# Optimization experiments

Measured on AMD Instinct MI355X. Metric: run time of the kernel, lower is better.

## Reference

```python
import jax, jax.numpy as jnp
import numpy as np

D_MODEL = 1024
NUM_HEADS = 16
HEAD_DIM = D_MODEL // NUM_HEADS
SCALE = 1.0 / float(np.sqrt(HEAD_DIM))


def setup_inputs() -> dict:
    key = jax.random.key(0)
    ks = jax.random.split(key, 9)
    B, S, D = 2, 2048, D_MODEL
    # Xavier-uniform bound for square (D, D) linear layers
    bound = float(np.sqrt(6.0 / (D + D)))
    def xavier(k):
        return jax.random.uniform(k, (D, D), jnp.float32, -bound, bound)
    return {
        "x": jax.random.normal(ks[0], (B, S, D), jnp.float32),
        "Wq": xavier(ks[1]), "bq": jnp.zeros((D,), jnp.float32),
        "Wk": xavier(ks[2]), "bk": jnp.zeros((D,), jnp.float32),
        "Wv": xavier(ks[3]), "bv": jnp.zeros((D,), jnp.float32),
        "Wo": xavier(ks[4]), "bo": jnp.zeros((D,), jnp.float32),
    }


def reference(x, Wq, bq, Wk, bk, Wv, bv, Wo, bo):
    B, S, D = x.shape
    H, Hd = NUM_HEADS, HEAD_DIM
    # torch Linear: y = x @ W.T + b
    def proj(W, b):
        y = jnp.einsum("bsd,ed->bse", x, W) + b
        return y.reshape(B, S, H, Hd).transpose(0, 2, 1, 3)  # (B,H,S,Hd)
    Q = proj(Wq, bq)
    K = proj(Wk, bk)
    V = proj(Wv, bv)
    # scaled scores (B,H,S,S) + additive causal mask (0 / -inf)
    scores = jnp.einsum("bhqd,bhkd->bhqk", Q, K) * SCALE
    causal = jnp.where(
        jnp.tril(jnp.ones((S, S), dtype=bool)), 0.0, -jnp.inf
    ).astype(scores.dtype)
    scores = scores + causal
    attn = jax.nn.softmax(scores, axis=-1)
    attn = jnp.nan_to_num(attn, nan=0.0)  # no-op here (causal rows never fully masked)
    # dropout p=0.0 -> identity
    ctx = jnp.einsum("bhqk,bhkd->bhqd", attn, V)  # (B,H,S,Hd)
    ctx = ctx.transpose(0, 2, 1, 3).reshape(B, S, D)
    out = jnp.einsum("bsd,ed->bse", ctx, Wo) + bo
    return out, attn
```

## Files before the change

### kernel.cpp

```cpp
#include <hip/hip_runtime.h>

typedef unsigned short u16;
using short8 = __attribute__((ext_vector_type(8))) short;
using f32x4  = __attribute__((ext_vector_type(4))) float;
using u16x4  = __attribute__((ext_vector_type(4))) unsigned short;

__device__ __forceinline__ u16 f2bf(float f) {
  union { float f; unsigned int u; } v; v.f = f;
  unsigned int u = v.u + 0x7FFFu + ((v.u >> 16) & 1u);
  return (u16)(u >> 16);
}
__device__ __forceinline__ float bf2f(u16 u) {
  union { unsigned int u; float f; } v; v.u = ((unsigned int)u) << 16;
  return v.f;
}
__device__ __forceinline__ void glds16(const void* g, void* l) {
  __builtin_amdgcn_global_load_lds(
      (const __attribute__((address_space(1))) void*)g,
      (__attribute__((address_space(3))) void*)l, 16, 0, 0);
}

__global__ __launch_bounds__(256) void cast_all(
    const float* __restrict__ x, const float* __restrict__ wq,
    const float* __restrict__ wk, const float* __restrict__ wv,
    const float* __restrict__ wo,
    u16* __restrict__ xb, u16* __restrict__ wqb, u16* __restrict__ wkb,
    u16* __restrict__ wvb, u16* __restrict__ wob) {
  int i = blockIdx.x * 256 + threadIdx.x;
  const float4* src; ushort4* dst; int off;
  if (i < 1048576)      { src = (const float4*)x;  dst = (ushort4*)xb;  off = i; }
  else if (i < 1310720) { src = (const float4*)wq; dst = (ushort4*)wqb; off = i - 1048576; }
  else if (i < 1572864) { src = (const float4*)wk; dst = (ushort4*)wkb; off = i - 1310720; }
  else if (i < 1835008) { src = (const float4*)wv; dst = (ushort4*)wvb; off = i - 1572864; }
  else                  { src = (const float4*)wo; dst = (ushort4*)wob; off = i - 1835008; }
  float4 v = src[off];
  ushort4 o;
  o.x = f2bf(v.x); o.y = f2bf(v.y); o.z = f2bf(v.z); o.w = f2bf(v.w);
  dst[off] = o;
}

template<int MODE>
__global__ __launch_bounds__(256) void gemm_nt_glds(
    const u16* __restrict__ A,
    const u16* __restrict__ B0, const u16* __restrict__ B1, const u16* __restrict__ B2,
    const float* __restrict__ bias0, const float* __restrict__ bias1, const float* __restrict__ bias2,
    void* __restrict__ C0, void* __restrict__ C1, void* __restrict__ C2,
    int K)
{
  __shared__ u16 smem[16896];
  u16* As = smem;
  u16* Bs = smem + 8192;
  const int bn = blockIdx.x, bm = blockIdx.y;
  const int sel = bn >> 3, bnl = bn & 7;
  const u16* B = sel == 0 ? B0 : (sel == 1 ? B1 : B2);
  const float* bias = sel == 0 ? bias0 : (sel == 1 ? bias1 : bias2);
  void* C = sel == 0 ? C0 : (sel == 1 ? C1 : C2);

  const int tid = threadIdx.x;
  const int w = tid >> 6, lane = tid & 63, quad = lane >> 4, l16 = lane & 15;
  const int wm = w >> 1, wn = w & 1;
  const int srow = lane >> 3, gc = (lane & 7) ^ srow;

  const u16* aseg = A + (size_t)(bm * 128 + w * 32 + srow) * K + gc * 8;
  const u16* bseg = B + (size_t)(bnl * 128 + w * 32 + srow) * K + gc * 8;

  const f32x4 z4 = {0.f, 0.f, 0.f, 0.f};
  f32x4 acc[4][4];
#pragma unroll
  for (int mt = 0; mt < 4; mt++)
#pragma unroll
    for (int nt = 0; nt < 4; nt++) acc[mt][nt] = z4;

  for (int k0 = 0; k0 < K; k0 += 64) {
    __syncthreads();
#pragma unroll
    for (int j = 0; j < 4; j++) {
      glds16(aseg + (size_t)(j * 8) * K + k0, As + (w * 4 + j) * 512);
      glds16(bseg + (size_t)(j * 8) * K + k0, Bs + (w * 4 + j) * 512);
    }
    __syncthreads();
#pragma unroll
    for (int ks = 0; ks < 2; ks++) {
      short8 af[4], bf[4];
#pragma unroll
      for (int mt = 0; mt < 4; mt++) {
        int row = wm * 64 + mt * 16 + l16;
        int chk = (ks * 4 + quad) ^ (row & 7);
        af[mt] = *(const short8*)((const short*)As + row * 64 + chk * 8);
      }
#pragma unroll
      for (int nt = 0; nt < 4; nt++) {
        int row = wn * 64 + nt * 16 + l16;
        int chk = (ks * 4 + quad) ^ (row & 7);
        bf[nt] = *(const short8*)((const short*)Bs + row * 64 + chk * 8);
      }
#pragma unroll
      for (int mt = 0; mt < 4; mt++)
#pragma unroll
        for (int nt = 0; nt < 4; nt++)
          acc[mt][nt] = __builtin_amdgcn_mfma_f32_16x16x32_bf16(af[mt], bf[nt], acc[mt][nt], 0, 0, 0);
    }
  }

  if (MODE == 0 && sel == 2) {
    __syncthreads();
#pragma unroll
    for (int mt = 0; mt < 4; mt++) {
      int r0 = wm * 64 + mt * 16 + quad * 4;
#pragma unroll
      for (int nt = 0; nt < 4; nt++) {
        int c = wn * 64 + nt * 16 + l16;
        float bvv = bias[bnl * 128 + c];
        u16x4 pk;
#pragma unroll
        for (int r = 0; r < 4; r++) pk[r] = f2bf(acc[mt][nt][r] + bvv);
        *(u16x4*)(smem + c * 132 + r0) = pk;
      }
    }
    __syncthreads();
    const int bb = bm >> 4;
    const size_t sb = (size_t)(bm & 15) * 128;
    u16* Cv = (u16*)C;
#pragma unroll
    for (int i = 0; i < 16; i++) {
      int idx = tid + i * 256;
      int dr = idx >> 5, c4 = (idx & 31) * 4;
      u16x4 v = *(const u16x4*)(smem + dr * 132 + c4);
      *(u16x4*)(Cv + ((size_t)bb * 1024 + bnl * 128 + dr) * 2048 + sb + c4) = v;
    }
  } else {
    const float cmul = (MODE == 0 && sel == 0) ? 0.125f : 1.0f;
#pragma unroll
    for (int mt = 0; mt < 4; mt++) {
      int row0 = bm * 128 + wm * 64 + mt * 16 + quad * 4;
#pragma unroll
      for (int nt = 0; nt < 4; nt++) {
        int col = bnl * 128 + wn * 64 + nt * 16 + l16;
        float bv = bias[col];
#pragma unroll
        for (int r = 0; r < 4; r++) {
          float v = (acc[mt][nt][r] + bv) * cmul;
          if (MODE) ((float*)C)[(size_t)(row0 + r) * 1024 + col] = v;
          else      ((u16*)C)[(size_t)(row0 + r) * 1024 + col] = f2bf(v);
        }
      }
    }
  }
}

__global__ __launch_bounds__(256) void attn_kernel(
    const u16* __restrict__ Qb, const u16* __restrict__ Kbuf,
    const u16* __restrict__ Vtb, float* __restrict__ attn,
    u16* __restrict__ ctx)
{
  __shared__ u16 Ks[2][128 * 64];
  __shared__ u16 Ps[128 * 128];
  __shared__ float ls[128];

  const int flat = blockIdx.x;
  const int half = flat >> 8, r0 = flat & 255;
  const int bh = (half << 4) | (r0 >> 4);
  const int qb = half ? (15 - (r0 & 15)) : (r0 & 15);
  const int b = bh >> 4, h = bh & 15;

  const int tid = threadIdx.x;
  const int w = tid >> 6, lane = tid & 63, quad = lane >> 4, l16 = lane & 15;
  const int wm = w >> 1, wn = w & 1;
  const int srow8 = lane >> 3, gc8 = (lane & 7) ^ srow8;
  const int srow16 = lane >> 4, sc16 = lane & 15;

  const int S = 2048, D = 1024;
  const u16* Qg = Qb + ((size_t)b * S + qb * 128) * D + h * 64;
  const u16* Kg = Kbuf + (size_t)b * S * D + h * 64;
  const u16* Vg = Vtb + ((size_t)b * D + h * 64) * S;
  float* attng = attn + ((size_t)(b * 16 + h) * S + qb * 128) * S;

  const f32x4 z4 = {0.f, 0.f, 0.f, 0.f};

#pragma unroll
  for (int j = 0; j < 4; j++)
    glds16(Qg + (size_t)(w * 32 + j * 8 + srow8) * D + gc8 * 8, (u16*)Ps + (w * 4 + j) * 512);
  if (tid < 128) ls[tid] = 0.f;
#pragma unroll
  for (int j = 0; j < 4; j++)
    glds16(Kg + (size_t)(w * 32 + j * 8 + srow8) * D + gc8 * 8, Ks[0] + (w * 4 + j) * 512);
  __syncthreads();

  short8 qf[4][2];
#pragma unroll
  for (int mt = 0; mt < 4; mt++) {
    int row = wm * 64 + mt * 16 + l16;
#pragma unroll
    for (int ks = 0; ks < 2; ks++) {
      int chk = (ks * 4 + quad) ^ (row & 7);
      qf[mt][ks] = *(const short8*)((const short*)Ps + row * 64 + chk * 8);
    }
  }

  float rowsum[4][4];
#pragma unroll
  for (int mt = 0; mt < 4; mt++)
#pragma unroll
    for (int rr = 0; rr < 4; rr++) rowsum[mt][rr] = 0.f;

  for (int kb = 0; kb <= qb; kb++) {
    if (kb) __syncthreads();
    if (kb < qb) {
#pragma unroll
      for (int j = 0; j < 4; j++)
        glds16(Kg + (size_t)((kb + 1) * 128 + w * 32 + j * 8 + srow8) * D + gc8 * 8,
               Ks[(kb + 1) & 1] + (w * 4 + j) * 512);
    }
    const u16* kbf = Ks[kb & 1];
    f32x4 acc[4][4];
#pragma unroll
    for (int mt = 0; mt < 4; mt++)
#pragma unroll
      for (int nt = 0; nt < 4; nt++) acc[mt][nt] = z4;
    __builtin_amdgcn_s_setprio(1);
#pragma unroll
    for (int ks = 0; ks < 2; ks++) {
      short8 bf[4];
#pragma unroll
      for (int nt = 0; nt < 4; nt++) {
        int row = wn * 64 + nt * 16 + l16;
        int chk = (ks * 4 + quad) ^ (row & 7);
        bf[nt] = *(const short8*)((const short*)kbf + row * 64 + chk * 8);
      }
#pragma unroll
      for (int mt = 0; mt < 4; mt++)
#pragma unroll
        for (int nt = 0; nt < 4; nt++)
          acc[mt][nt] = __builtin_amdgcn_mfma_f32_16x16x32_bf16(qf[mt][ks], bf[nt], acc[mt][nt], 0, 0, 0);
    }
    __builtin_amdgcn_s_setprio(0);
    if (kb < qb) {
#pragma unroll
      for (int mt = 0; mt < 4; mt++)
#pragma unroll
        for (int rr = 0; rr < 4; rr++) {
          float s = 0.f;
#pragma unroll
          for (int nt = 0; nt < 4; nt++)
            s += __expf(fminf(acc[mt][nt][rr], 30.f));
          rowsum[mt][rr] += s;
        }
    } else {
#pragma unroll
      for (int mt = 0; mt < 4; mt++)
#pragma unroll
        for (int rr = 0; rr < 4; rr++) {
          int rloc = wm * 64 + mt * 16 + quad * 4 + rr;
          float s = 0.f;
#pragma unroll
          for (int nt = 0; nt < 4; nt++) {
            int ck = wn * 64 + nt * 16 + l16;
            s += (ck <= rloc) ? __expf(fminf(acc[mt][nt][rr], 30.f)) : 0.f;
          }
          rowsum[mt][rr] += s;
        }
    }
  }

#pragma unroll
  for (int mt = 0; mt < 4; mt++)
#pragma unroll
    for (int rr = 0; rr < 4; rr++) {
      float s = rowsum[mt][rr];
      s += __shfl_xor(s, 1);
      s += __shfl_xor(s, 2);
      s += __shfl_xor(s, 4);
      s += __shfl_xor(s, 8);
      if (l16 == 0) atomicAdd(&ls[wm * 64 + mt * 16 + quad * 4 + rr], s);
    }
  __syncthreads();
  float rl[4][4];
#pragma unroll
  for (int mt = 0; mt < 4; mt++)
#pragma unroll
    for (int rr = 0; rr < 4; rr++)
      rl[mt][rr] = 1.0f / ls[wm * 64 + mt * 16 + quad * 4 + rr];

#pragma unroll
  for (int j = 0; j < 4; j++)
    glds16(Kg + (size_t)(w * 32 + j * 8 + srow8) * D + gc8 * 8, Ks[0] + (w * 4 + j) * 512);

  f32x4 cacc[2][4];
#pragma unroll
  for (int mt = 0; mt < 2; mt++)
#pragma unroll
    for (int nt = 0; nt < 4; nt++) cacc[mt][nt] = z4;

  for (int kb = 0; kb <= qb; kb++) {
    __syncthreads();
#pragma unroll
    for (int j = 0; j < 4; j++) {
      int r0v = (w * 4 + j) * 4;
      int row = r0v + srow16;
      int gcv = sc16 ^ (row & 7);
      glds16(Vg + (size_t)row * S + kb * 128 + gcv * 8, Ks[1] + r0v * 128);
    }
    f32x4 acc[4][4];
#pragma unroll
    for (int mt = 0; mt < 4; mt++)
#pragma unroll
      for (int nt = 0; nt < 4; nt++) acc[mt][nt] = z4;
    __builtin_amdgcn_s_setprio(1);
#pragma unroll
    for (int ks = 0; ks < 2; ks++) {
      short8 bf[4];
#pragma unroll
      for (int nt = 0; nt < 4; nt++) {
        int row = wn * 64 + nt * 16 + l16;
        int chk = (ks * 4 + quad) ^ (row & 7);
        bf[nt] = *(const short8*)((const short*)Ks[0] + row * 64 + chk * 8);
      }
#pragma unroll
      for (int mt = 0; mt < 4; mt++)
#pragma unroll
        for (int nt = 0; nt < 4; nt++)
          acc[mt][nt] = __builtin_amdgcn_mfma_f32_16x16x32_bf16(qf[mt][ks], bf[nt], acc[mt][nt], 0, 0, 0);
    }
    __builtin_amdgcn_s_setprio(0);
    bool diag = (kb == qb);
#pragma unroll
    for (int mt = 0; mt < 4; mt++)
#pragma unroll
      for (int rr = 0; rr < 4; rr++) {
        int rloc = wm * 64 + mt * 16 + quad * 4 + rr;
        float rlv = rl[mt][rr];
#pragma unroll
        for (int nt = 0; nt < 4; nt++) {
          int colk = wn * 64 + nt * 16 + l16;
          float e = __expf(fminf(acc[mt][nt][rr], 30.f)) * rlv;
          if (diag && colk > rloc) e = 0.f;
          Ps[rloc * 128 + (((colk >> 3) ^ (rloc & 7)) << 3) + (colk & 7)] = f2bf(e);
        }
      }
    __syncthreads();
    if (kb < qb) {
#pragma unroll
      for (int j = 0; j < 4; j++)
        glds16(Kg + (size_t)((kb + 1) * 128 + w * 32 + j * 8 + srow8) * D + gc8 * 8,
               Ks[0] + (w * 4 + j) * 512);
    }
#pragma unroll
    for (int s = 0; s < 16; s++) {
      int e4 = s * 256 + tid;
      int row = e4 >> 5, col = (e4 & 31) * 4;
      int chunk = (col >> 3) ^ (row & 7);
      u16x4 pv = *(const u16x4*)((const u16*)Ps + row * 128 + chunk * 8 + (col & 7));
      f32x4 o;
      o[0] = bf2f(pv[0]); o[1] = bf2f(pv[1]); o[2] = bf2f(pv[2]); o[3] = bf2f(pv[3]);
      __builtin_nontemporal_store(o, (f32x4*)(attng + (size_t)row * S + kb * 128 + col));
    }
    __builtin_amdgcn_s_setprio(1);
#pragma unroll
    for (int ks = 0; ks < 4; ks++) {
      short8 pf[2], vf[4];
#pragma unroll
      for (int mt = 0; mt < 2; mt++) {
        int row = w * 32 + mt * 16 + l16;
        int chk = (ks * 4 + quad) ^ (row & 7);
        pf[mt] = *(const short8*)((const short*)Ps + row * 128 + chk * 8);
      }
#pragma unroll
      for (int nt = 0; nt < 4; nt++) {
        int row = nt * 16 + l16;
        int chk = (ks * 4 + quad) ^ (row & 7);
        vf[nt] = *(const short8*)((const short*)Ks[1] + row * 128 + chk * 8);
      }
#pragma unroll
      for (int mt = 0; mt < 2; mt++)
#pragma unroll
        for (int nt = 0; nt < 4; nt++)
          cacc[mt][nt] = __builtin_amdgcn_mfma_f32_16x16x32_bf16(pf[mt], vf[nt], cacc[mt][nt], 0, 0, 0);
    }
    __builtin_amdgcn_s_setprio(0);
  }

  {
    int kstart = (qb + 1) * 128;
    const f32x4 zz = {0.f, 0.f, 0.f, 0.f};
    for (int rr = 0; rr < 128; rr++) {
      float* rowp = attng + (size_t)rr * S;
      for (int c = kstart + tid * 4; c < S; c += 1024)
        __builtin_nontemporal_store(zz, (f32x4*)(rowp + c));
    }
  }

#pragma unroll
  for (int mt = 0; mt < 2; mt++)
#pragma unroll
    for (int nt = 0; nt < 4; nt++)
#pragma unroll
      for (int rr = 0; rr < 4; rr++) {
        int row_local = w * 32 + mt * 16 + quad * 4 + rr;
        int col = nt * 16 + l16;
        ctx[((size_t)b * S + qb * 128 + row_local) * D + h * 64 + col] = f2bf(cacc[mt][nt][rr]);
      }
}

extern "C" void kernel_launch(void* const* d_in, const int* in_sizes, int n_in,
                              void* d_out, int out_size, void* d_ws, size_t ws_size,
                              hipStream_t stream) {
  const float* x  = (const float*)d_in[0];
  const float* Wq = (const float*)d_in[1];
  const float* bq = (const float*)d_in[2];
  const float* Wk = (const float*)d_in[3];
  const float* bk = (const float*)d_in[4];
  const float* Wv = (const float*)d_in[5];
  const float* bv = (const float*)d_in[6];
  const float* Wo = (const float*)d_in[7];
  const float* bo = (const float*)d_in[8];

  float* out_f32  = (float*)d_out;
  float* attn_out = (float*)d_out + 4194304;

  char* w = (char*)d_ws;
  u16* xb   = (u16*)(w + 0);
  u16* Wqb  = (u16*)(w + 8388608);
  u16* Wkb  = (u16*)(w + 10485760);
  u16* Wvb  = (u16*)(w + 12582912);
  u16* Wob  = (u16*)(w + 14680064);
  u16* Qbuf = (u16*)(w + 16777216);
  u16* Kbuf = (u16*)(w + 25165824);
  u16* Vtb  = (u16*)(w + 41943040);
  u16* ctxb = (u16*)(w + 50331648);

  cast_all<<<8192, 256, 0, stream>>>(x, Wq, Wk, Wv, Wo, xb, Wqb, Wkb, Wvb, Wob);

  gemm_nt_glds<0><<<dim3(24, 32), 256, 0, stream>>>(
      xb, Wqb, Wkb, Wvb, bq, bk, bv, Qbuf, Kbuf, Vtb, 1024);

  attn_kernel<<<512, 256, 0, stream>>>(Qbuf, Kbuf, Vtb, attn_out, ctxb);

  gemm_nt_glds<1><<<dim3(8, 32), 256, 0, stream>>>(
      ctxb, Wob, Wob, Wob, bo, bo, bo, out_f32, out_f32, out_f32, 1024);
}
```

Measured before the change: 713.8 us.

## Double attention block to 512 threads and remap blocks to balance causal work per XCD

The attention kernel now launches 512 threads per block with 8 waves, each wave owning 32 query rows in the score phase (4x2 wave grid) and 16 rows in the PV phase. Per-wave accumulators and loads are halved, which lowers register pressure and aims to raise latency hiding within each 128-row query tile. Block indices are also remapped so that blocks landing on the same XCD (flat & 7) get a balanced mix of ascending and descending causal tiles from the same heads. In exchange, synchronisation involves more waves, and MFMA work per LDS fragment load drops.

Measured after the change: 775.6 us. 1.09x slower.

```diff
diff --git a/kernel.cpp b/kernel.cpp
--- a/kernel.cpp
+++ b/kernel.cpp
@@ -148,7 +148,7 @@
   }
 }
 
-__global__ __launch_bounds__(256) void attn_kernel(
+__global__ __launch_bounds__(512, 4) void attn_kernel(
     const u16* __restrict__ Qb, const u16* __restrict__ Kbuf,
     const u16* __restrict__ Vtb, float* __restrict__ attn,
     u16* __restrict__ ctx)
@@ -158,9 +158,10 @@
   __shared__ float ls[128];
 
   const int flat = blockIdx.x;
-  const int half = flat >> 8, r0 = flat & 255;
-  const int bh = (half << 4) | (r0 >> 4);
-  const int qb = half ? (15 - (r0 & 15)) : (r0 & 15);
+  const int x = flat & 7, slot = flat >> 3;
+  int bh, qb;
+  if (slot < 32) { bh = x * 4 + (slot >> 4);            qb = slot & 15; }
+  else           { bh = x * 4 + 2 + ((slot - 32) >> 4); qb = 15 - ((slot - 32) & 15); }
   const int b = bh >> 4, h = bh & 15;
 
   const int tid = threadIdx.x;
@@ -178,18 +179,18 @@
   const f32x4 z4 = {0.f, 0.f, 0.f, 0.f};
 
 #pragma unroll
-  for (int j = 0; j < 4; j++)
-    glds16(Qg + (size_t)(w * 32 + j * 8 + srow8) * D + gc8 * 8, (u16*)Ps + (w * 4 + j) * 512);
+  for (int j = 0; j < 2; j++)
+    glds16(Qg + (size_t)(w * 16 + j * 8 + srow8) * D + gc8 * 8, (u16*)Ps + (w * 2 + j) * 512);
   if (tid < 128) ls[tid] = 0.f;
 #pragma unroll
-  for (int j = 0; j < 4; j++)
-    glds16(Kg + (size_t)(w * 32 + j * 8 + srow8) * D + gc8 * 8, Ks[0] + (w * 4 + j) * 512);
+  for (int j = 0; j < 2; j++)
+    glds16(Kg + (size_t)(w * 16 + j * 8 + srow8) * D + gc8 * 8, Ks[0] + (w * 2 + j) * 512);
   __syncthreads();
 
-  short8 qf[4][2];
-#pragma unroll
-  for (int mt = 0; mt < 4; mt++) {
-    int row = wm * 64 + mt * 16 + l16;
+  short8 qf[2][2];
+#pragma unroll
+  for (int mt = 0; mt < 2; mt++) {
+    int row = wm * 32 + mt * 16 + l16;
 #pragma unroll
     for (int ks = 0; ks < 2; ks++) {
       int chk = (ks * 4 + quad) ^ (row & 7);
@@ -197,9 +198,9 @@
     }
   }
 
-  float rowsum[4][4];
-#pragma unroll
-  for (int mt = 0; mt < 4; mt++)
+  float rowsum[2][4];
+#pragma unroll
+  for (int mt = 0; mt < 2; mt++)
 #pragma unroll
     for (int rr = 0; rr < 4; rr++) rowsum[mt][rr] = 0.f;
 
@@ -207,14 +208,14 @@
     if (kb) __syncthreads();
     if (kb < qb) {
 #pragma unroll
-      for (int j = 0; j < 4; j++)
-        glds16(Kg + (size_t)((kb + 1) * 128 + w * 32 + j * 8 + srow8) * D + gc8 * 8,
-               Ks[(kb + 1) & 1] + (w * 4 + j) * 512);
+      for (int j = 0; j < 2; j++)
+        glds16(Kg + (size_t)((kb + 1) * 128 + w * 16 + j * 8 + srow8) * D + gc8 * 8,
+               Ks[(kb + 1) & 1] + (w * 2 + j) * 512);
     }
     const u16* kbf = Ks[kb & 1];
-    f32x4 acc[4][4];
-#pragma unroll
-    for (int mt = 0; mt < 4; mt++)
+    f32x4 acc[2][4];
+#pragma unroll
+    for (int mt = 0; mt < 2; mt++)
 #pragma unroll
       for (int nt = 0; nt < 4; nt++) acc[mt][nt] = z4;
     __builtin_amdgcn_s_setprio(1);
@@ -228,7 +229,7 @@
         bf[nt] = *(const short8*)((const short*)kbf + row * 64 + chk * 8);
       }
 #pragma unroll
-      for (int mt = 0; mt < 4; mt++)
+      for (int mt = 0; mt < 2; mt++)
 #pragma unroll
         for (int nt = 0; nt < 4; nt++)
           acc[mt][nt] = __builtin_amdgcn_mfma_f32_16x16x32_bf16(qf[mt][ks], bf[nt], acc[mt][nt], 0, 0, 0);
@@ -236,7 +237,7 @@
     __builtin_amdgcn_s_setprio(0);
     if (kb < qb) {
 #pragma unroll
-      for (int mt = 0; mt < 4; mt++)
+      for (int mt = 0; mt < 2; mt++)
 #pragma unroll
         for (int rr = 0; rr < 4; rr++) {
           float s = 0.f;
@@ -247,10 +248,10 @@
         }
     } else {
 #pragma unroll
-      for (int mt = 0; mt < 4; mt++)
+      for (int mt = 0; mt < 2; mt++)
 #pragma unroll
         for (int rr = 0; rr < 4; rr++) {
-          int rloc = wm * 64 + mt * 16 + quad * 4 + rr;
+          int rloc = wm * 32 + mt * 16 + quad * 4 + rr;
           float s = 0.f;
 #pragma unroll
           for (int nt = 0; nt < 4; nt++) {
@@ -263,7 +264,7 @@
   }
 
 #pragma unroll
-  for (int mt = 0; mt < 4; mt++)
+  for (int mt = 0; mt < 2; mt++)
 #pragma unroll
     for (int rr = 0; rr < 4; rr++) {
       float s = rowsum[mt][rr];
@@ -271,38 +272,36 @@
       s += __shfl_xor(s, 2);
       s += __shfl_xor(s, 4);
       s += __shfl_xor(s, 8);
-      if (l16 == 0) atomicAdd(&ls[wm * 64 + mt * 16 + quad * 4 + rr], s);
+      if (l16 == 0) atomicAdd(&ls[wm * 32 + mt * 16 + quad * 4 + rr], s);
     }
   __syncthreads();
-  float rl[4][4];
-#pragma unroll
-  for (int mt = 0; mt < 4; mt++)
+  float rl[2][4];
+#pragma unroll
+  for (int mt = 0; mt < 2; mt++)
 #pragma unroll
     for (int rr = 0; rr < 4; rr++)
-      rl[mt][rr] = 1.0f / ls[wm * 64 + mt * 16 + quad * 4 + rr];
-
-#pragma unroll
-  for (int j = 0; j < 4; j++)
-    glds16(Kg + (size_t)(w * 32 + j * 8 + srow8) * D + gc8 * 8, Ks[0] + (w * 4 + j) * 512);
-
-  f32x4 cacc[2][4];
-#pragma unroll
-  for (int mt = 0; mt < 2; mt++)
-#pragma unroll
-    for (int nt = 0; nt < 4; nt++) cacc[mt][nt] = z4;
+      rl[mt][rr] = 1.0f / ls[wm * 32 + mt * 16 + quad * 4 + rr];
+
+#pragma unroll
+  for (int j = 0; j < 2; j++)
+    glds16(Kg + (size_t)(w * 16 + j * 8 + srow8) * D + gc8 * 8, Ks[0] + (w * 2 + j) * 512);
+
+  f32x4 cacc[4];
+#pragma unroll
+  for (int nt = 0; nt < 4; nt++) cacc[nt] = z4;
 
   for (int kb = 0; kb <= qb; kb++) {
     __syncthreads();
 #pragma unroll
-    for (int j = 0; j < 4; j++) {
-      int r0v = (w * 4 + j) * 4;
+    for (int j = 0; j < 2; j++) {
+      int r0v = (w * 2 + j) * 4;
       int row = r0v + srow16;
       int gcv = sc16 ^ (row & 7);
       glds16(Vg + (size_t)row * S + kb * 128 + gcv * 8, Ks[1] + r0v * 128);
     }
-    f32x4 acc[4][4];
-#pragma unroll
-    for (int mt = 0; mt < 4; mt++)
+    f32x4 acc[2][4];
+#pragma unroll
+    for (int mt = 0; mt < 2; mt++)
 #pragma unroll
       for (int nt = 0; nt < 4; nt++) acc[mt][nt] = z4;
     __builtin_amdgcn_s_setprio(1);
@@ -316,7 +315,7 @@
         bf[nt] = *(const short8*)((const short*)Ks[0] + row * 64 + chk * 8);
       }
 #pragma unroll
-      for (int mt = 0; mt < 4; mt++)
+      for (int mt = 0; mt < 2; mt++)
 #pragma unroll
         for (int nt = 0; nt < 4; nt++)
           acc[mt][nt] = __builtin_amdgcn_mfma_f32_16x16x32_bf16(qf[mt][ks], bf[nt], acc[mt][nt], 0, 0, 0);
@@ -324,10 +323,10 @@
     __builtin_amdgcn_s_setprio(0);
     bool diag = (kb == qb);
 #pragma unroll
-    for (int mt = 0; mt < 4; mt++)
+    for (int mt = 0; mt < 2; mt++)
 #pragma unroll
       for (int rr = 0; rr < 4; rr++) {
-        int rloc = wm * 64 + mt * 16 + quad * 4 + rr;
+        int rloc = wm * 32 + mt * 16 + quad * 4 + rr;
         float rlv = rl[mt][rr];
 #pragma unroll
         for (int nt = 0; nt < 4; nt++) {
@@ -340,13 +339,13 @@
     __syncthreads();
     if (kb < qb) {
 #pragma unroll
-      for (int j = 0; j < 4; j++)
-        glds16(Kg + (size_t)((kb + 1) * 128 + w * 32 + j * 8 + srow8) * D + gc8 * 8,
-               Ks[0] + (w * 4 + j) * 512);
-    }
-#pragma unroll
-    for (int s = 0; s < 16; s++) {
-      int e4 = s * 256 + tid;
+      for (int j = 0; j < 2; j++)
+        glds16(Kg + (size_t)((kb + 1) * 128 + w * 16 + j * 8 + srow8) * D + gc8 * 8,
+               Ks[0] + (w * 2 + j) * 512);
+    }
+#pragma unroll
+    for (int s = 0; s < 8; s++) {
+      int e4 = s * 512 + tid;
       int row = e4 >> 5, col = (e4 & 31) * 4;
       int chunk = (col >> 3) ^ (row & 7);
       u16x4 pv = *(const u16x4*)((const u16*)Ps + row * 128 + chunk * 8 + (col & 7));
@@ -357,12 +356,11 @@
     __builtin_amdgcn_s_setprio(1);
 #pragma unroll
     for (int ks = 0; ks < 4; ks++) {
-      short8 pf[2], vf[4];
-#pragma unroll
-      for (int mt = 0; mt < 2; mt++) {
-        int row = w * 32 + mt * 16 + l16;
-        int chk = (ks * 4 + quad) ^ (row & 7);
-        pf[mt] = *(const short8*)((const short*)Ps + row * 128 + chk * 8);
+      short8 pf, vf[4];
+      {
+        int row = w * 16 + l16;
+        int chk = (ks * 4 + quad) ^ (row & 7);
+        pf = *(const short8*)((const short*)Ps + row * 128 + chk * 8);
       }
 #pragma unroll
       for (int nt = 0; nt < 4; nt++) {
@@ -371,10 +369,8 @@
         vf[nt] = *(const short8*)((const short*)Ks[1] + row * 128 + chk * 8);
       }
 #pragma unroll
-      for (int mt = 0; mt < 2; mt++)
-#pragma unroll
-        for (int nt = 0; nt < 4; nt++)
-          cacc[mt][nt] = __builtin_amdgcn_mfma_f32_16x16x32_bf16(pf[mt], vf[nt], cacc[mt][nt], 0, 0, 0);
+      for (int nt = 0; nt < 4; nt++)
+        cacc[nt] = __builtin_amdgcn_mfma_f32_16x16x32_bf16(pf, vf[nt], cacc[nt], 0, 0, 0);
     }
     __builtin_amdgcn_s_setprio(0);
   }
@@ -384,21 +380,19 @@
     const f32x4 zz = {0.f, 0.f, 0.f, 0.f};
     for (int rr = 0; rr < 128; rr++) {
       float* rowp = attng + (size_t)rr * S;
-      for (int c = kstart + tid * 4; c < S; c += 1024)
+      for (int c = kstart + tid * 4; c < S; c += 2048)
         __builtin_nontemporal_store(zz, (f32x4*)(rowp + c));
     }
   }
 
 #pragma unroll
-  for (int mt = 0; mt < 2; mt++)
-#pragma unroll
-    for (int nt = 0; nt < 4; nt++)
-#pragma unroll
-      for (int rr = 0; rr < 4; rr++) {
-        int row_local = w * 32 + mt * 16 + quad * 4 + rr;
-        int col = nt * 16 + l16;
-        ctx[((size_t)b * S + qb * 128 + row_local) * D + h * 64 + col] = f2bf(cacc[mt][nt][rr]);
-      }
+  for (int nt = 0; nt < 4; nt++)
+#pragma unroll
+    for (int rr = 0; rr < 4; rr++) {
+      int row_local = w * 16 + quad * 4 + rr;
+      int col = nt * 16 + l16;
+      ctx[((size_t)b * S + qb * 128 + row_local) * D + h * 64 + col] = f2bf(cacc[nt][rr]);
+    }
 }
 
 extern "C" void kernel_launch(void* const* d_in, const int* in_sizes, int n_in,
@@ -433,7 +427,7 @@
   gemm_nt_glds<0><<<dim3(24, 32), 256, 0, stream>>>(
       xb, Wqb, Wkb, Wvb, bq, bk, bv, Qbuf, Kbuf, Vtb, 1024);
 
-  attn_kernel<<<512, 256, 0, stream>>>(Qbuf, Kbuf, Vtb, attn_out, ctxb);
+  attn_kernel<<<512, 512, 0, stream>>>(Qbuf, Kbuf, Vtb, attn_out, ctxb);
 
   gemm_nt_glds<1><<<dim3(8, 32), 256, 0, stream>>>(
       ctxb, Wob, Wob, Wob, bo, bo, bo, out_f32, out_f32, out_f32, 1024);
```
